# Kernel tuning notes

Measured on AMD Instinct MI355X. Metric: run time of the kernel, lower is better.

Reference implementation:

```python
import jax, jax.numpy as jnp
import numpy as np

B, S, E, H = 1, 2048, 2048, 16
D = E // H  # head_dim = 128
EPS = 1e-6
NEG_INF = -1e30


def _rms_norm(x, gamma):
    # RMSNorm over last dim: x / sqrt(mean(x^2)+eps) * gamma
    return x * jax.lax.rsqrt(jnp.mean(x * x, axis=-1, keepdims=True) + EPS) * gamma


def _rotate_half(x):
    x1, x2 = jnp.split(x, 2, axis=-1)
    return jnp.concatenate([-x2, x1], axis=-1)


def _rope(x, cos, sin):
    # x: [B,H,S,D]; cos/sin: [S,D] broadcast over batch and heads
    return x * cos + _rotate_half(x) * sin


def setup_inputs() -> dict:
    key = jax.random.key(0)
    ks = jax.random.split(key, 5)
    sc = lambda n: 1.0 / np.sqrt(n)
    x = jax.random.normal(ks[0], (B, S, E), jnp.float32)
    # realistic RoPE tables
    inv_freq = 1.0 / (10000.0 ** (jnp.arange(0, D, 2, dtype=jnp.float32) / D))
    t = jnp.arange(S, dtype=jnp.float32)
    freqs = jnp.outer(t, inv_freq)                    # [S, D/2]
    emb = jnp.concatenate([freqs, freqs], axis=-1)    # [S, D]
    cos, sin = jnp.cos(emb), jnp.sin(emb)
    Wq = jax.random.normal(ks[1], (E, E), jnp.float32) * sc(E)
    Wk = jax.random.normal(ks[2], (D, E), jnp.float32) * sc(E)
    Wv = jax.random.normal(ks[3], (D, E), jnp.float32) * sc(E)
    Wo = jax.random.normal(ks[4], (E, E), jnp.float32) * sc(E)
    q_gamma = jnp.ones((D,), jnp.float32)
    k_gamma = jnp.ones((D,), jnp.float32)
    return dict(x=x, cos=cos, sin=sin, Wq=Wq, Wk=Wk, Wv=Wv, Wo=Wo,
                q_gamma=q_gamma, k_gamma=k_gamma)


def reference(x, cos, sin, Wq, Wk, Wv, Wo, q_gamma, k_gamma):
    # projections (Linear with bias=False -> x @ W.T)
    Q = (x @ Wq.T).reshape(B, S, H, D).transpose(0, 2, 1, 3)  # [B,H,S,D]
    K = (x @ Wk.T)[:, None, :, :]                             # [B,1,S,D]
    V = x @ Wv.T                                              # [B,S,D] (single KV head)
    # qk-norm
    Q = _rms_norm(Q, q_gamma)
    K = _rms_norm(K, k_gamma)  # computed then discarded below (faithful to source)
    # RoPE — source bug replicated: K is overwritten with roped Q
    Q = _rope(Q, cos, sin)
    K = _rope(Q, cos, sin)     # [B,H,S,D]
    # causal attention (dense stand-in for flash_attn_func, scale 1/sqrt(D))
    scores = jnp.einsum('bhqd,bhkd->bhqk', Q, K) / jnp.sqrt(jnp.float32(D))
    causal = jnp.tril(jnp.ones((S, S), bool))
    scores = jnp.where(causal, scores, NEG_INF)
    probs = jax.nn.softmax(scores, axis=-1)
    # single V head broadcast across query heads
    out = jnp.einsum('bhqk,bkd->bqhd', probs, V).reshape(B, S, E)
    return out @ Wo.T
```

## Files before the change

### kernel.cpp

```cpp
#include <hip/hip_runtime.h>
#include <hip/hip_bf16.h>

#define SL 2048
#define NH 16
#define HD 128
#define EMB 2048

typedef __attribute__((ext_vector_type(8))) __bf16 bf16x8;
typedef __attribute__((ext_vector_type(4))) float f32x4;
typedef __attribute__((ext_vector_type(8))) short short8;

__device__ __forceinline__ short bf16bits(float x) {
  union { __hip_bfloat16 h; short s; } u;
  u.h = __float2bfloat16(x);
  return u.s;
}

#define GLDS16(gp, lp) __builtin_amdgcn_global_load_lds( \
    (__attribute__((address_space(1))) void*)(gp), \
    (__attribute__((address_space(3))) void*)(lp), 16, 0, 0)

__global__ __launch_bounds__(256) void cast_f32_bf16(const float* __restrict__ in,
                                                     short* __restrict__ out, int n) {
  int i = (blockIdx.x * 256 + threadIdx.x) * 8;
  if (i >= n) return;
  float4 a = *(const float4*)(in + i);
  float4 b = *(const float4*)(in + i + 4);
  short8 o;
  o[0] = bf16bits(a.x); o[1] = bf16bits(a.y); o[2] = bf16bits(a.z); o[3] = bf16bits(a.w);
  o[4] = bf16bits(b.x); o[5] = bf16bits(b.y); o[6] = bf16bits(b.z); o[7] = bf16bits(b.w);
  *(short8*)(out + i) = o;
}

template<int MODE>
__global__ __launch_bounds__(512, 1) void gemm128(const short* __restrict__ A,
                                                  const short* __restrict__ B,
                                                  float* __restrict__ C,
                                                  short* __restrict__ Qb,
                                                  short* __restrict__ Kb,
                                                  const float* __restrict__ cosT,
                                                  const float* __restrict__ sinT,
                                                  const float* __restrict__ gamma) {
  __shared__ char arena[131072];
  short* As = (short*)arena;
  const int K = 2048;
  int id = blockIdx.x;
  int nid = (id & 7) * 32 + (id >> 3);
  int tn = nid >> 4, tm = nid & 15;
  int tid = threadIdx.x;
  int w = tid >> 6, lane = tid & 63;
  int g = lane >> 4, c = lane & 15;
  int wr = w >> 2, wc = w & 3;
  const short* Ab = A + (long)(tm * 128) * K;
  const short* Bb = B + (long)(tn * 128) * K;
  int lr = lane >> 3;
  int lsw = (lane & 7) ^ lr;
  f32x4 zero = {0.f, 0.f, 0.f, 0.f};
  f32x4 acc[4][2];
#pragma unroll
  for (int m = 0; m < 4; ++m)
#pragma unroll
    for (int n = 0; n < 2; ++n) acc[m][n] = zero;

#define STG(buf, kt) do { \
    _Pragma("unroll") \
    for (int j = 0; j < 2; ++j) { \
      int rb = w * 16 + j * 8; \
      GLDS16(Ab + (long)(rb + lr) * K + (kt) + lsw * 8, \
             As + (buf) * 16384 + rb * 64); \
      GLDS16(Bb + (long)(rb + lr) * K + (kt) + lsw * 8, \
             As + (buf) * 16384 + 8192 + rb * 64); \
    } } while (0)

  STG(0, 0);
  STG(1, 64);
  STG(2, 128);
  asm volatile("s_waitcnt vmcnt(8)" ::: "memory");
  __builtin_amdgcn_s_barrier();

  for (int it = 0; it < 32; ++it) {
    int bf = it & 3;
    if (it < 29) STG((it + 3) & 3, (it + 3) * 64);
    const short* Ax = As + bf * 16384;
    const short* Bx = Ax + 8192;
    bf16x8 af[2][4], bfr[2][2];
#pragma unroll
    for (int kk = 0; kk < 2; ++kk) {
      int ch = ((kk * 4 + g) ^ (c & 7)) * 8;
#pragma unroll
      for (int m = 0; m < 4; ++m)
        af[kk][m] = *(const bf16x8*)(Ax + (wr * 64 + m * 16 + c) * 64 + ch);
#pragma unroll
      for (int n = 0; n < 2; ++n)
        bfr[kk][n] = *(const bf16x8*)(Bx + (wc * 32 + n * 16 + c) * 64 + ch);
    }
    __builtin_amdgcn_s_setprio(1);
#pragma unroll
    for (int kk = 0; kk < 2; ++kk)
#pragma unroll
      for (int m = 0; m < 4; ++m)
#pragma unroll
        for (int n = 0; n < 2; ++n)
          acc[m][n] = __builtin_amdgcn_mfma_f32_16x16x32_bf16(af[kk][m], bfr[kk][n],
                                                              acc[m][n], 0, 0, 0);
    __builtin_amdgcn_s_setprio(0);
    if (it < 29) {
      asm volatile("s_waitcnt vmcnt(8)" ::: "memory");
    } else if (it == 29) {
      asm volatile("s_waitcnt vmcnt(4)" ::: "memory");
    } else if (it == 30) {
      asm volatile("s_waitcnt vmcnt(0)" ::: "memory");
    }
    if (it < 31) __builtin_amdgcn_s_barrier();
  }
#undef STG

  if constexpr (MODE == 0) {
#pragma unroll
    for (int m = 0; m < 4; ++m)
#pragma unroll
      for (int n = 0; n < 2; ++n)
#pragma unroll
        for (int r = 0; r < 4; ++r) {
          int row = tm * 128 + wr * 64 + m * 16 + g * 4 + r;
          int col = tn * 128 + wc * 32 + n * 16 + c;
          C[(long)row * 2048 + col] = acc[m][n][r];
        }
  } else {
    float* xch = (float*)arena;
    float* ssb = (float*)(arena + 65536);
    float ssmr[4][4];
#pragma unroll
    for (int m = 0; m < 4; ++m)
#pragma unroll
      for (int r = 0; r < 4; ++r) {
        float s = acc[m][0][r] * acc[m][0][r] + acc[m][1][r] * acc[m][1][r];
#pragma unroll
        for (int off = 1; off <= 8; off <<= 1) s += __shfl_xor(s, off, 64);
        ssmr[m][r] = s;
      }
    if (c == 0) {
#pragma unroll
      for (int m = 0; m < 4; ++m)
#pragma unroll
        for (int r = 0; r < 4; ++r)
          ssb[wc * 128 + wr * 64 + m * 16 + g * 4 + r] = ssmr[m][r];
    }
#pragma unroll
    for (int m = 0; m < 4; ++m)
#pragma unroll
      for (int n = 0; n < 2; ++n)
#pragma unroll
        for (int r = 0; r < 4; ++r)
          xch[(wr * 64 + m * 16 + g * 4 + r) * 128 + wc * 32 + n * 16 + c] = acc[m][n][r];
    __syncthreads();
    float rn[4][4];
#pragma unroll
    for (int m = 0; m < 4; ++m)
#pragma unroll
      for (int r = 0; r < 4; ++r) {
        int rl = wr * 64 + m * 16 + g * 4 + r;
        float s4 = ssb[rl] + ssb[128 + rl] + ssb[256 + rl] + ssb[384 + rl];
        rn[m][r] = rsqrtf(s4 * (1.0f / 128.0f) + 1e-6f);
      }
    float sgn = (wc < 2) ? -1.f : 1.f;
    float g_own[2], g_par[2];
#pragma unroll
    for (int n = 0; n < 2; ++n) {
      int d = wc * 32 + n * 16 + c;
      g_own[n] = gamma[d];
      g_par[n] = gamma[d ^ 64];
    }
#pragma unroll
    for (int m = 0; m < 4; ++m)
#pragma unroll
      for (int n = 0; n < 2; ++n)
#pragma unroll
        for (int r = 0; r < 4; ++r) {
          int rl = wr * 64 + m * 16 + g * 4 + r;
          int s = tm * 128 + rl;
          int d = wc * 32 + n * 16 + c;
          int u = (wc & 1) * 32 + n * 16 + c;
          float cv = cosT[s * 128 + u];
          float sv = sinT[s * 128 + u];
          float xo = acc[m][n][r] * rn[m][r] * g_own[n];
          float xq = xch[rl * 128 + (d ^ 64)] * rn[m][r] * g_par[n];
          float y  = xo * cv + sgn * xq * sv;
          float yp = xq * cv - sgn * xo * sv;
          float kk = y * cv + sgn * yp * sv;
          long o = ((long)tn * SL + s) * HD + d;
          Qb[o] = bf16bits(y);
          Kb[o] = bf16bits(kk);
        }
  }
}

template<int MODE>
__global__ __launch_bounds__(256, 3) void gemm64(const short* __restrict__ A,
                                                 const short* __restrict__ B,
                                                 short* __restrict__ VT) {
  __shared__ char lds_raw[36864];
  short* As = (short*)lds_raw;
  short* Bs = (short*)(lds_raw + 12288);
  const int K = 2048;
  int nwg = gridDim.x;
  int id = blockIdx.x;
  int nid = (id & 7) * (nwg >> 3) + (id >> 3);
  int tn = 16;
  int tm = nid & 31;
  int tid = threadIdx.x;
  int wave = tid >> 6, lane = tid & 63;
  int g = lane >> 4, c = lane & 15;
  int wr = wave >> 1, wc = wave & 1;
  const short* Ab = A + (long)(tm * 64) * K;
  const short* Bb = B + (long)(tn * 128) * K;
  int swz = (lane & 3) ^ ((lane >> 3) & 3);
  int rdc = (g ^ ((c >> 1) & 3)) * 8;
  f32x4 zero = {0.f, 0.f, 0.f, 0.f};
  f32x4 acc[2][4];
#pragma unroll
  for (int m = 0; m < 2; ++m)
#pragma unroll
    for (int n = 0; n < 4; ++n) acc[m][n] = zero;

#define STG(buf, kt) do { \
    GLDS16(Ab + (long)(wave * 16 + (lane >> 2)) * K + (kt) + swz * 8, \
           As + (buf) * 2048 + wave * 512); \
    _Pragma("unroll") \
    for (int hh = 0; hh < 2; ++hh) { \
      int rb = wave * 32 + hh * 16; \
      GLDS16(Bb + (long)(rb + (lane >> 2)) * K + (kt) + swz * 8, \
             Bs + (buf) * 4096 + rb * 32); \
    } } while (0)

  STG(0, 0);
  STG(1, 32);
  asm volatile("s_waitcnt vmcnt(3)" ::: "memory");
  __builtin_amdgcn_s_barrier();

  int b0 = 0, b1 = 1, b2 = 2;
  for (int it = 0; it < 64; ++it) {
    if (it < 62) STG(b2, (it + 2) * 32);
    bf16x8 a[2], b[4];
#pragma unroll
    for (int m = 0; m < 2; ++m)
      a[m] = *(const bf16x8*)(As + b0 * 2048 + (wr * 32 + m * 16 + c) * 32 + rdc);
#pragma unroll
    for (int n = 0; n < 4; ++n)
      b[n] = *(const bf16x8*)(Bs + b0 * 4096 + (wc * 64 + n * 16 + c) * 32 + rdc);
    __builtin_amdgcn_s_setprio(1);
#pragma unroll
    for (int m = 0; m < 2; ++m)
#pragma unroll
      for (int n = 0; n < 4; ++n)
        acc[m][n] = __builtin_amdgcn_mfma_f32_16x16x32_bf16(a[m], b[n], acc[m][n], 0, 0, 0);
    __builtin_amdgcn_s_setprio(0);
    if (it < 62) {
      asm volatile("s_waitcnt vmcnt(3)" ::: "memory");
      __builtin_amdgcn_s_barrier();
    } else if (it == 62) {
      asm volatile("s_waitcnt vmcnt(0)" ::: "memory");
      __builtin_amdgcn_s_barrier();
    }
    int t = b0; b0 = b1; b1 = b2; b2 = t;
  }
#undef STG

#pragma unroll
  for (int m = 0; m < 2; ++m)
#pragma unroll
    for (int n = 0; n < 4; ++n)
#pragma unroll
      for (int r = 0; r < 4; ++r) {
        int s = tm * 64 + wr * 32 + m * 16 + g * 4 + r;
        int d = wc * 64 + n * 16 + c;
        VT[(long)d * SL + s] = bf16bits(acc[m][n][r]);
      }
}

__global__ __launch_bounds__(256, 2) void attn_part(const short* __restrict__ Qb,
                                                    const short* __restrict__ Kb,
                                                    const short* __restrict__ VTg,
                                                    short* __restrict__ att,
                                                    float* __restrict__ pO,
                                                    float* __restrict__ pml) {
  __shared__ short Ks[2][64 * 128];
  __shared__ short Vs[2][128 * 64];
  __shared__ short Ps[4][16 * 72];
  int wave = threadIdx.x >> 6, lane = threadIdx.x & 63;
  int g = lane >> 4, c = lane & 15;
  int h = blockIdx.y;
  int x = blockIdx.x & 15;
  int cbk = blockIdx.x >> 4;
  const short* Qh = Qb + (long)h * SL * HD;
  const short* Kh = Kb + (long)h * SL * HD;
  f32x4 zero = {0.f, 0.f, 0.f, 0.f};
  const float sc = 0.08838834764831845f;

  int pqt[2], plo[2], pcnt[2], pout[2];
  if (cbk == 0) {
    pqt[0] = x;      plo[0] = 0;      pcnt[0] = x + 1;  pout[0] = 0;
    pqt[1] = 31 - x; plo[1] = 0;      pcnt[1] = 16 - x; pout[1] = 1;
  } else {
    pqt[0] = 31 - x; plo[0] = 16 - x; pcnt[0] = 16;     pout[0] = 2;
    pqt[1] = 0;      plo[1] = 0;      pcnt[1] = 0;      pout[1] = 0;
  }
  int total = pcnt[0] + pcnt[1];

#define ASTAGE(b, kvb) do { \
    _Pragma("unroll") \
    for (int i = 0; i < 4; ++i) { \
      int rb = wave * 16 + i * 4; \
      int row = rb + (lane >> 4); \
      int c16 = (lane & 15) ^ (row & 7); \
      GLDS16(Kh + (long)((kvb) + row) * HD + c16 * 8, &Ks[b][rb * 128]); \
    } \
    _Pragma("unroll") \
    for (int i = 0; i < 4; ++i) { \
      int dbase = i * 32 + wave * 8; \
      int drow = dbase + (lane >> 3); \
      int u8 = (lane & 7) ^ (drow & 7); \
      GLDS16(VTg + (long)drow * SL + (kvb) + u8 * 8, &Vs[b][dbase * 64]); \
    } } while (0)

  ASTAGE(0, plo[0] * 64);
  int s = 0;

  for (int p = 0; p < 2; ++p) {
    int nt = pcnt[p];
    if (nt == 0) break;
    int qt = pqt[p];
    int qb = qt * 64 + wave * 16;
    int qown = qb + c;

    bf16x8 aq[4];
#pragma unroll
    for (int kc = 0; kc < 4; ++kc)
      aq[kc] = *(const bf16x8*)(Qh + (long)qown * HD + kc * 32 + g * 8);

    float m = -1e30f, l = 0.f;
    f32x4 O[8];
#pragma unroll
    for (int d8 = 0; d8 < 8; ++d8) O[d8] = zero;

    for (int i = 0; i < nt; ++i, ++s) {
      int kt = plo[p] + i;
      int kvb = kt * 64;
      int bcu = s & 1;
      asm volatile("s_waitcnt vmcnt(0)" ::: "memory");
      __builtin_amdgcn_s_barrier();
      {
        int ns = s + 1;
        if (ns < total) {
          int np = (ns < pcnt[0]) ? 0 : 1;
          int nkt = plo[np] + (ns - (np ? pcnt[0] : 0));
          ASTAGE(bcu ^ 1, nkt * 64);
        }
      }

      f32x4 sf[4];
#pragma unroll
      for (int n = 0; n < 4; ++n) sf[n] = zero;
      __builtin_amdgcn_s_setprio(1);
#pragma unroll
      for (int kc = 0; kc < 4; ++kc)
#pragma unroll
        for (int n = 0; n < 4; ++n) {
          int row = n * 16 + c;
          int u = (kc * 4 + g) ^ (row & 7);
          bf16x8 bk = *(const bf16x8*)(&Ks[bcu][row * 128 + u * 8]);
          sf[n] = __builtin_amdgcn_mfma_f32_16x16x32_bf16(bk, aq[kc], sf[n], 0, 0, 0);
        }
      __builtin_amdgcn_s_setprio(0);

      float pm = -1e30f;
      if (kt == qt) {
#pragma unroll
        for (int n = 0; n < 4; ++n) {
#pragma unroll
          for (int r = 0; r < 4; ++r) {
            int k = kvb + n * 16 + g * 4 + r;
            float v = sf[n][r] * sc;
            if (k > qown) v = -1e30f;
            sf[n][r] = v;
          }
          float a0 = fmaxf(sf[n][0], sf[n][1]);
          float a1 = fmaxf(sf[n][2], sf[n][3]);
          pm = fmaxf(pm, fmaxf(a0, a1));
        }
      } else {
#pragma unroll
        for (int n = 0; n < 4; ++n) {
#pragma unroll
          for (int r = 0; r < 4; ++r) sf[n][r] *= sc;
          float a0 = fmaxf(sf[n][0], sf[n][1]);
          float a1 = fmaxf(sf[n][2], sf[n][3]);
          pm = fmaxf(pm, fmaxf(a0, a1));
        }
      }
      pm = fmaxf(pm, __shfl_xor(pm, 16, 64));
      pm = fmaxf(pm, __shfl_xor(pm, 32, 64));

      if (__any(pm > m + 8.f)) {
        float mn_ = fmaxf(m, pm);
        float corr = __expf(m - mn_);
        m = mn_;
        l *= corr;
        float c4[4];
#pragma unroll
        for (int r = 0; r < 4; ++r) c4[r] = __shfl(corr, g * 4 + r, 64);
#pragma unroll
        for (int d8 = 0; d8 < 8; ++d8)
#pragma unroll
          for (int r = 0; r < 4; ++r) O[d8][r] *= c4[r];
      }

#pragma unroll
      for (int n = 0; n < 4; ++n)
#pragma unroll
        for (int hh = 0; hh < 2; ++hh) {
          float p0 = __expf(sf[n][2 * hh + 0] - m);
          float p1 = __expf(sf[n][2 * hh + 1] - m);
          l += p0 + p1;
          unsigned pk = (unsigned)(unsigned short)bf16bits(p0) |
                        ((unsigned)(unsigned short)bf16bits(p1) << 16);
          *(unsigned*)&Ps[wave][c * 72 + n * 16 + g * 4 + 2 * hh] = pk;
        }

#pragma unroll
      for (int k2 = 0; k2 < 2; ++k2) {
        bf16x8 ap = *(const bf16x8*)(&Ps[wave][c * 72 + k2 * 32 + g * 8]);
        __builtin_amdgcn_s_setprio(1);
#pragma unroll
        for (int d8 = 0; d8 < 8; ++d8) {
          int drow = d8 * 16 + c;
          int u = (k2 * 4 + g) ^ (c & 7);
          bf16x8 bv = *(const bf16x8*)(&Vs[bcu][drow * 64 + u * 8]);
          O[d8] = __builtin_amdgcn_mfma_f32_16x16x32_bf16(ap, bv, O[d8], 0, 0, 0);
        }
        __builtin_amdgcn_s_setprio(0);
      }
    }

    if (pout[p] == 0) {
      float lf = l;
      lf += __shfl_xor(lf, 16, 64);
      lf += __shfl_xor(lf, 32, 64);
      float rinv = 1.0f / lf;
      float r4[4];
#pragma unroll
      for (int r = 0; r < 4; ++r) r4[r] = __shfl(rinv, g * 4 + r, 64);
#pragma unroll
      for (int d8 = 0; d8 < 8; ++d8)
#pragma unroll
        for (int r = 0; r < 4; ++r) {
          int q = qb + g * 4 + r;
          att[(long)q * EMB + h * HD + d8 * 16 + c] = bf16bits(O[d8][r] * r4[r]);
        }
    } else {
      int part = pout[p] - 1;
      float lf = l;
      lf += __shfl_xor(lf, 16, 64);
      lf += __shfl_xor(lf, 32, 64);
      float* Op = pO + ((long)(part * 16 + x) * 16 + h) * 8192;
#pragma unroll
      for (int d8 = 0; d8 < 8; ++d8)
#pragma unroll
        for (int r = 0; r < 4; ++r)
          Op[(wave * 16 + g * 4 + r) * 128 + d8 * 16 + c] = O[d8][r];
      if (g == 0) {
        float* pmb = pml + ((part * 16 + x) * 16 + h) * 64 + wave * 16 + c;
        pmb[0]     = m;
        pmb[32768] = lf;
      }
    }
  }
#undef ASTAGE
}

__global__ __launch_bounds__(256) void attn_comb(const float* __restrict__ pO,
                                                 const float* __restrict__ pml,
                                                 short* __restrict__ att) {
  int b = blockIdx.x;
  int x = b & 15, h = b >> 4;
  int qt = 31 - x;
  int t = threadIdx.x;
  int q = t >> 2, d0 = (t & 3) * 32;
  int i0 = (x * 16 + h) * 64 + q;
  int i1 = (256 + x * 16 + h) * 64 + q;
  float m0 = pml[i0], m1 = pml[i1];
  float l0 = pml[32768 + i0], l1 = pml[32768 + i1];
  float M = fmaxf(m0, m1);
  float w0 = __expf(m0 - M), w1 = __expf(m1 - M);
  float inv = 1.0f / (l0 * w0 + l1 * w1);
  const float* O0 = pO + ((long)(x * 16 + h)) * 8192 + q * 128 + d0;
  const float* O1 = pO + ((long)(256 + x * 16 + h)) * 8192 + q * 128 + d0;
  short* out = att + (long)(qt * 64 + q) * EMB + h * HD + d0;
#pragma unroll
  for (int j = 0; j < 32; j += 4) {
    float4 a = *(const float4*)(O0 + j);
    float4 bb = *(const float4*)(O1 + j);
    out[j + 0] = bf16bits((a.x * w0 + bb.x * w1) * inv);
    out[j + 1] = bf16bits((a.y * w0 + bb.y * w1) * inv);
    out[j + 2] = bf16bits((a.z * w0 + bb.z * w1) * inv);
    out[j + 3] = bf16bits((a.w * w0 + bb.w * w1) * inv);
  }
}

extern "C" void kernel_launch(void* const* d_in, const int* in_sizes, int n_in,
                              void* d_out, int out_size, void* d_ws, size_t ws_size,
                              hipStream_t stream) {
  const float* x    = (const float*)d_in[0];
  const float* cosT = (const float*)d_in[1];
  const float* sinT = (const float*)d_in[2];
  const float* Wq   = (const float*)d_in[3];
  const float* Wv   = (const float*)d_in[5];
  const float* Wo   = (const float*)d_in[6];
  const float* qg   = (const float*)d_in[7];

  char* w = (char*)d_ws;
  short* xb   = (short*)(w + 0);
  short* wqvb = (short*)(w + 8388608);
  short* wob  = (short*)(w + 17301504);
  short* vt   = (short*)(w + 25690112);
  short* qb   = (short*)(w + 26214400);
  short* kb   = (short*)(w + 34603008);
  short* attb = (short*)(w + 42991616);
  float* pO   = (float*)(w + 0);
  float* pml  = (float*)(w + 16777216);

  cast_f32_bf16<<<dim3(2048), dim3(256), 0, stream>>>(x,  xb,   4194304);
  cast_f32_bf16<<<dim3(2048), dim3(256), 0, stream>>>(Wq, wqvb, 4194304);
  cast_f32_bf16<<<dim3(128),  dim3(256), 0, stream>>>(Wv, wqvb + 4194304, 262144);
  cast_f32_bf16<<<dim3(2048), dim3(256), 0, stream>>>(Wo, wob,  4194304);

  gemm128<1><<<dim3(256), dim3(512), 0, stream>>>(xb, wqvb, nullptr, qb, kb,
                                                  cosT, sinT, qg);
  gemm64<2><<<dim3(32), dim3(256), 0, stream>>>(xb, wqvb, vt);
  attn_part<<<dim3(32, 16), dim3(256), 0, stream>>>(qb, kb, vt, attb, pO, pml);
  attn_comb<<<dim3(256), dim3(256), 0, stream>>>(pO, pml, attb);
  gemm128<0><<<dim3(256), dim3(512), 0, stream>>>(attb, wob, (float*)d_out,
                                                  nullptr, nullptr,
                                                  nullptr, nullptr, nullptr);
}
```

Before: 136.3 us.

## Fuse casts into one launch and fold V projection into QKV GEMM

Merges the four fp32-to-bf16 cast launches into one kernel that picks its source by index range. Removes the separate 64-row V GEMM by widening the Q GEMM grid to 272 tiles, so tile column 16 writes transposed V instead of running the norm/RoPE epilogue. Also remaps the attention grid to 1D with heads interleaved across block IDs, likely to spread work across XCDs. Together these cut launch overhead and let V compute overlap Q, but the 272-block grid is no longer a multiple of the CU count, which may leave a tail wave.

```diff
diff --git a/kernel.cpp b/kernel.cpp
--- a/kernel.cpp
+++ b/kernel.cpp
@@ -20,16 +20,25 @@
     (__attribute__((address_space(1))) void*)(gp), \
     (__attribute__((address_space(3))) void*)(lp), 16, 0, 0)
 
-__global__ __launch_bounds__(256) void cast_f32_bf16(const float* __restrict__ in,
-                                                     short* __restrict__ out, int n) {
-  int i = (blockIdx.x * 256 + threadIdx.x) * 8;
-  if (i >= n) return;
-  float4 a = *(const float4*)(in + i);
-  float4 b = *(const float4*)(in + i + 4);
+__global__ __launch_bounds__(256) void cast_all(const float* __restrict__ x,
+                                                const float* __restrict__ Wq,
+                                                const float* __restrict__ Wv,
+                                                const float* __restrict__ Wo,
+                                                short* __restrict__ xb,
+                                                short* __restrict__ wqvb,
+                                                short* __restrict__ wob) {
+  long i = ((long)blockIdx.x * 256 + threadIdx.x) * 8;
+  const float* in; short* out; long off;
+  if (i < 4194304)      { in = x;  out = xb;             off = i; }
+  else if (i < 8388608) { in = Wq; out = wqvb;           off = i - 4194304; }
+  else if (i < 8650752) { in = Wv; out = wqvb + 4194304; off = i - 8388608; }
+  else                  { in = Wo; out = wob;            off = i - 8650752; }
+  float4 a = *(const float4*)(in + off);
+  float4 b = *(const float4*)(in + off + 4);
   short8 o;
   o[0] = bf16bits(a.x); o[1] = bf16bits(a.y); o[2] = bf16bits(a.z); o[3] = bf16bits(a.w);
   o[4] = bf16bits(b.x); o[5] = bf16bits(b.y); o[6] = bf16bits(b.z); o[7] = bf16bits(b.w);
-  *(short8*)(out + i) = o;
+  *(short8*)(out + off) = o;
 }
 
 template<int MODE>
@@ -38,14 +47,16 @@
                                                   float* __restrict__ C,
                                                   short* __restrict__ Qb,
                                                   short* __restrict__ Kb,
+                                                  short* __restrict__ VT,
                                                   const float* __restrict__ cosT,
                                                   const float* __restrict__ sinT,
                                                   const float* __restrict__ gamma) {
   __shared__ char arena[131072];
   short* As = (short*)arena;
   const int K = 2048;
+  int nwg = gridDim.x;
   int id = blockIdx.x;
-  int nid = (id & 7) * 32 + (id >> 3);
+  int nid = (id & 7) * (nwg >> 3) + (id >> 3);
   int tn = nid >> 4, tm = nid & 15;
   int tid = threadIdx.x;
   int w = tid >> 6, lane = tid & 63;
@@ -127,155 +138,85 @@
           C[(long)row * 2048 + col] = acc[m][n][r];
         }
   } else {
-    float* xch = (float*)arena;
-    float* ssb = (float*)(arena + 65536);
-    float ssmr[4][4];
-#pragma unroll
-    for (int m = 0; m < 4; ++m)
-#pragma unroll
-      for (int r = 0; r < 4; ++r) {
-        float s = acc[m][0][r] * acc[m][0][r] + acc[m][1][r] * acc[m][1][r];
-#pragma unroll
-        for (int off = 1; off <= 8; off <<= 1) s += __shfl_xor(s, off, 64);
-        ssmr[m][r] = s;
-      }
-    if (c == 0) {
-#pragma unroll
-      for (int m = 0; m < 4; ++m)
-#pragma unroll
-        for (int r = 0; r < 4; ++r)
-          ssb[wc * 128 + wr * 64 + m * 16 + g * 4 + r] = ssmr[m][r];
-    }
-#pragma unroll
-    for (int m = 0; m < 4; ++m)
-#pragma unroll
-      for (int n = 0; n < 2; ++n)
-#pragma unroll
-        for (int r = 0; r < 4; ++r)
-          xch[(wr * 64 + m * 16 + g * 4 + r) * 128 + wc * 32 + n * 16 + c] = acc[m][n][r];
-    __syncthreads();
-    float rn[4][4];
-#pragma unroll
-    for (int m = 0; m < 4; ++m)
-#pragma unroll
-      for (int r = 0; r < 4; ++r) {
-        int rl = wr * 64 + m * 16 + g * 4 + r;
-        float s4 = ssb[rl] + ssb[128 + rl] + ssb[256 + rl] + ssb[384 + rl];
-        rn[m][r] = rsqrtf(s4 * (1.0f / 128.0f) + 1e-6f);
-      }
-    float sgn = (wc < 2) ? -1.f : 1.f;
-    float g_own[2], g_par[2];
-#pragma unroll
-    for (int n = 0; n < 2; ++n) {
-      int d = wc * 32 + n * 16 + c;
-      g_own[n] = gamma[d];
-      g_par[n] = gamma[d ^ 64];
-    }
-#pragma unroll
-    for (int m = 0; m < 4; ++m)
-#pragma unroll
-      for (int n = 0; n < 2; ++n)
+    if (tn == 16) {
+#pragma unroll
+      for (int m = 0; m < 4; ++m)
+#pragma unroll
+        for (int n = 0; n < 2; ++n)
+#pragma unroll
+          for (int r = 0; r < 4; ++r) {
+            int s = tm * 128 + wr * 64 + m * 16 + g * 4 + r;
+            int d = wc * 32 + n * 16 + c;
+            VT[(long)d * SL + s] = bf16bits(acc[m][n][r]);
+          }
+    } else {
+      float* xch = (float*)arena;
+      float* ssb = (float*)(arena + 65536);
+      float ssmr[4][4];
+#pragma unroll
+      for (int m = 0; m < 4; ++m)
+#pragma unroll
+        for (int r = 0; r < 4; ++r) {
+          float s = acc[m][0][r] * acc[m][0][r] + acc[m][1][r] * acc[m][1][r];
+#pragma unroll
+          for (int off = 1; off <= 8; off <<= 1) s += __shfl_xor(s, off, 64);
+          ssmr[m][r] = s;
+        }
+      if (c == 0) {
+#pragma unroll
+        for (int m = 0; m < 4; ++m)
+#pragma unroll
+          for (int r = 0; r < 4; ++r)
+            ssb[wc * 128 + wr * 64 + m * 16 + g * 4 + r] = ssmr[m][r];
+      }
+#pragma unroll
+      for (int m = 0; m < 4; ++m)
+#pragma unroll
+        for (int n = 0; n < 2; ++n)
+#pragma unroll
+          for (int r = 0; r < 4; ++r)
+            xch[(wr * 64 + m * 16 + g * 4 + r) * 128 + wc * 32 + n * 16 + c] = acc[m][n][r];
+      __syncthreads();
+      float rn[4][4];
+#pragma unroll
+      for (int m = 0; m < 4; ++m)
 #pragma unroll
         for (int r = 0; r < 4; ++r) {
           int rl = wr * 64 + m * 16 + g * 4 + r;
-          int s = tm * 128 + rl;
-          int d = wc * 32 + n * 16 + c;
-          int u = (wc & 1) * 32 + n * 16 + c;
-          float cv = cosT[s * 128 + u];
-          float sv = sinT[s * 128 + u];
-          float xo = acc[m][n][r] * rn[m][r] * g_own[n];
-          float xq = xch[rl * 128 + (d ^ 64)] * rn[m][r] * g_par[n];
-          float y  = xo * cv + sgn * xq * sv;
-          float yp = xq * cv - sgn * xo * sv;
-          float kk = y * cv + sgn * yp * sv;
-          long o = ((long)tn * SL + s) * HD + d;
-          Qb[o] = bf16bits(y);
-          Kb[o] = bf16bits(kk);
-        }
+          float s4 = ssb[rl] + ssb[128 + rl] + ssb[256 + rl] + ssb[384 + rl];
+          rn[m][r] = rsqrtf(s4 * (1.0f / 128.0f) + 1e-6f);
+        }
+      float sgn = (wc < 2) ? -1.f : 1.f;
+      float g_own[2], g_par[2];
+#pragma unroll
+      for (int n = 0; n < 2; ++n) {
+        int d = wc * 32 + n * 16 + c;
+        g_own[n] = gamma[d];
+        g_par[n] = gamma[d ^ 64];
+      }
+#pragma unroll
+      for (int m = 0; m < 4; ++m)
+#pragma unroll
+        for (int n = 0; n < 2; ++n)
+#pragma unroll
+          for (int r = 0; r < 4; ++r) {
+            int rl = wr * 64 + m * 16 + g * 4 + r;
+            int s = tm * 128 + rl;
+            int d = wc * 32 + n * 16 + c;
+            int u = (wc & 1) * 32 + n * 16 + c;
+            float cv = cosT[s * 128 + u];
+            float sv = sinT[s * 128 + u];
+            float xo = acc[m][n][r] * rn[m][r] * g_own[n];
+            float xq = xch[rl * 128 + (d ^ 64)] * rn[m][r] * g_par[n];
+            float y  = xo * cv + sgn * xq * sv;
+            float yp = xq * cv - sgn * xo * sv;
+            float kk = y * cv + sgn * yp * sv;
+            long o = ((long)tn * SL + s) * HD + d;
+            Qb[o] = bf16bits(y);
+            Kb[o] = bf16bits(kk);
+          }
+    }
   }
-}
-
-template<int MODE>
-__global__ __launch_bounds__(256, 3) void gemm64(const short* __restrict__ A,
-                                                 const short* __restrict__ B,
-                                                 short* __restrict__ VT) {
-  __shared__ char lds_raw[36864];
-  short* As = (short*)lds_raw;
-  short* Bs = (short*)(lds_raw + 12288);
-  const int K = 2048;
-  int nwg = gridDim.x;
-  int id = blockIdx.x;
-  int nid = (id & 7) * (nwg >> 3) + (id >> 3);
-  int tn = 16;
-  int tm = nid & 31;
-  int tid = threadIdx.x;
-  int wave = tid >> 6, lane = tid & 63;
-  int g = lane >> 4, c = lane & 15;
-  int wr = wave >> 1, wc = wave & 1;
-  const short* Ab = A + (long)(tm * 64) * K;
-  const short* Bb = B + (long)(tn * 128) * K;
-  int swz = (lane & 3) ^ ((lane >> 3) & 3);
-  int rdc = (g ^ ((c >> 1) & 3)) * 8;
-  f32x4 zero = {0.f, 0.f, 0.f, 0.f};
-  f32x4 acc[2][4];
-#pragma unroll
-  for (int m = 0; m < 2; ++m)
-#pragma unroll
-    for (int n = 0; n < 4; ++n) acc[m][n] = zero;
-
-#define STG(buf, kt) do { \
-    GLDS16(Ab + (long)(wave * 16 + (lane >> 2)) * K + (kt) + swz * 8, \
-           As + (buf) * 2048 + wave * 512); \
-    _Pragma("unroll") \
-    for (int hh = 0; hh < 2; ++hh) { \
-      int rb = wave * 32 + hh * 16; \
-      GLDS16(Bb + (long)(rb + (lane >> 2)) * K + (kt) + swz * 8, \
-             Bs + (buf) * 4096 + rb * 32); \
-    } } while (0)
-
-  STG(0, 0);
-  STG(1, 32);
-  asm volatile("s_waitcnt vmcnt(3)" ::: "memory");
-  __builtin_amdgcn_s_barrier();
-
-  int b0 = 0, b1 = 1, b2 = 2;
-  for (int it = 0; it < 64; ++it) {
-    if (it < 62) STG(b2, (it + 2) * 32);
-    bf16x8 a[2], b[4];
-#pragma unroll
-    for (int m = 0; m < 2; ++m)
-      a[m] = *(const bf16x8*)(As + b0 * 2048 + (wr * 32 + m * 16 + c) * 32 + rdc);
-#pragma unroll
-    for (int n = 0; n < 4; ++n)
-      b[n] = *(const bf16x8*)(Bs + b0 * 4096 + (wc * 64 + n * 16 + c) * 32 + rdc);
-    __builtin_amdgcn_s_setprio(1);
-#pragma unroll
-    for (int m = 0; m < 2; ++m)
-#pragma unroll
-      for (int n = 0; n < 4; ++n)
-        acc[m][n] = __builtin_amdgcn_mfma_f32_16x16x32_bf16(a[m], b[n], acc[m][n], 0, 0, 0);
-    __builtin_amdgcn_s_setprio(0);
-    if (it < 62) {
-      asm volatile("s_waitcnt vmcnt(3)" ::: "memory");
-      __builtin_amdgcn_s_barrier();
-    } else if (it == 62) {
-      asm volatile("s_waitcnt vmcnt(0)" ::: "memory");
-      __builtin_amdgcn_s_barrier();
-    }
-    int t = b0; b0 = b1; b1 = b2; b2 = t;
-  }
-#undef STG
-
-#pragma unroll
-  for (int m = 0; m < 2; ++m)
-#pragma unroll
-    for (int n = 0; n < 4; ++n)
-#pragma unroll
-      for (int r = 0; r < 4; ++r) {
-        int s = tm * 64 + wr * 32 + m * 16 + g * 4 + r;
-        int d = wc * 64 + n * 16 + c;
-        VT[(long)d * SL + s] = bf16bits(acc[m][n][r]);
-      }
 }
 
 __global__ __launch_bounds__(256, 2) void attn_part(const short* __restrict__ Qb,
@@ -289,9 +230,10 @@
   __shared__ short Ps[4][16 * 72];
   int wave = threadIdx.x >> 6, lane = threadIdx.x & 63;
   int g = lane >> 4, c = lane & 15;
-  int h = blockIdx.y;
-  int x = blockIdx.x & 15;
-  int cbk = blockIdx.x >> 4;
+  int id = blockIdx.x;
+  int h = ((id & 7) << 1) | (id >> 8);
+  int x = (id >> 3) & 15;
+  int cbk = (id >> 7) & 1;
   const short* Qh = Qb + (long)h * SL * HD;
   const short* Kh = Kb + (long)h * SL * HD;
   f32x4 zero = {0.f, 0.f, 0.f, 0.f};
@@ -529,17 +471,13 @@
   float* pO   = (float*)(w + 0);
   float* pml  = (float*)(w + 16777216);
 
-  cast_f32_bf16<<<dim3(2048), dim3(256), 0, stream>>>(x,  xb,   4194304);
-  cast_f32_bf16<<<dim3(2048), dim3(256), 0, stream>>>(Wq, wqvb, 4194304);
-  cast_f32_bf16<<<dim3(128),  dim3(256), 0, stream>>>(Wv, wqvb + 4194304, 262144);
-  cast_f32_bf16<<<dim3(2048), dim3(256), 0, stream>>>(Wo, wob,  4194304);
-
-  gemm128<1><<<dim3(256), dim3(512), 0, stream>>>(xb, wqvb, nullptr, qb, kb,
+  cast_all<<<dim3(6272), dim3(256), 0, stream>>>(x, Wq, Wv, Wo, xb, wqvb, wob);
+
+  gemm128<1><<<dim3(272), dim3(512), 0, stream>>>(xb, wqvb, nullptr, qb, kb, vt,
                                                   cosT, sinT, qg);
-  gemm64<2><<<dim3(32), dim3(256), 0, stream>>>(xb, wqvb, vt);
-  attn_part<<<dim3(32, 16), dim3(256), 0, stream>>>(qb, kb, vt, attb, pO, pml);
+  attn_part<<<dim3(512), dim3(256), 0, stream>>>(qb, kb, vt, attb, pO, pml);
   attn_comb<<<dim3(256), dim3(256), 0, stream>>>(pO, pml, attb);
   gemm128<0><<<dim3(256), dim3(512), 0, stream>>>(attb, wob, (float*)d_out,
-                                                  nullptr, nullptr,
+                                                  nullptr, nullptr, nullptr,
                                                   nullptr, nullptr, nullptr);
 }
```

Result: faster. 130.2 us (-4.5%).
